# Kernel tuning notes

Hardware: AMD Instinct MI355X
Metric: run time of the kernel (lower is better)

The kernel has to match this reference:

```python
import jax, jax.numpy as jnp
import numpy as np


def setup_inputs() -> dict:
    key = jax.random.key(0)
    k1, k2 = jax.random.split(key)
    B, C, H, W = 16, 3, 512, 512
    predicted = jax.random.normal(k1, (B, C, H, W), dtype=jnp.float32)
    target = jax.random.randint(k2, (B, H, W), 0, 3, dtype=jnp.int32)
    return {"predicted": predicted, "target": target, "num_classes": 3}


def reference(predicted, target, num_classes):
    # predicted: [B, C, H, W] logits; target: [B, H, W] int labels
    B, C, H, W = predicted.shape
    smooth = 1.0

    # F.cross_entropy with default 'mean' reduction over all pixels
    logp = jax.nn.log_softmax(predicted, axis=1)           # [B,C,H,W]
    ce = -jnp.mean(jnp.take_along_axis(logp, target[:, None, :, :], axis=1))

    # Dice: the original casts softmax probs with .long() before summing,
    # which truncates toward zero (probs in [0,1) -> 0, exactly 1.0 -> 1).
    # We reproduce that faithfully with jnp.trunc.
    probs = jnp.exp(logp).reshape(B, C, H * W)             # softmax probs, [B,C,HW]
    tp = jnp.trunc(probs)                                   # faithful to .long() cast
    tgt = target.reshape(B, H * W)
    onehot = (tgt[:, None, :] == jnp.arange(num_classes)[None, :, None]).astype(probs.dtype)  # [B,nc,HW]

    intersection = jnp.sum(tp[:, :num_classes, :] * onehot, axis=-1)                 # [B,nc]
    union = jnp.sum(tp[:, :num_classes, :], axis=-1) + jnp.sum(onehot, axis=-1)      # [B,nc]
    coef = (2.0 * intersection + smooth) / (union + smooth)                           # [B,nc]
    batch_dice = jnp.mean(coef)  # mean over classes then batch == mean over both

    return ce + 1.0 - batch_dice
```

## Files before the change

### kernel.cpp

```cpp
#include <hip/hip_runtime.h>

constexpr int B_   = 16;
constexpr int C_   = 3;
constexpr int HW_  = 512 * 512;
constexpr int THREADS = 256;
constexpr int BLOCKS_PER_IMG = 128;
constexpr int NBLOCKS = B_ * BLOCKS_PER_IMG;
constexpr int F4_PER_BLOCK = HW_ / 4 / BLOCKS_PER_IMG;
constexpr int ITERS = F4_PER_BLOCK / THREADS;
constexpr int REC = 8;


__global__ __launch_bounds__(THREADS) void dice_ce_partial(
    const float* __restrict__ pred, const int* __restrict__ tgt,
    float* __restrict__ ws) {
  const int b = blockIdx.x / BLOCKS_PER_IMG;
  const int j = blockIdx.x % BLOCKS_PER_IMG;
  const int t = threadIdx.x;

  const float4* p0 = (const float4*)(pred + (size_t)b * C_ * HW_);
  const float4* p1 = (const float4*)(pred + (size_t)b * C_ * HW_ + HW_);
  const float4* p2 = (const float4*)(pred + (size_t)b * C_ * HW_ + 2 * HW_);
  const int4*   tg = (const int4*)(tgt + (size_t)b * HW_);

  float4 A0[ITERS], A1[ITERS], A2[ITERS];
  int4   T[ITERS];
#pragma unroll
  for (int i = 0; i < ITERS; ++i) {
    const int idx = j * F4_PER_BLOCK + i * THREADS + t;
    A0[i] = p0[idx];
    A1[i] = p1[idx];
    A2[i] = p2[idx];
    T[i]  = tg[idx];
  }

  float ce = 0.f;
  int pkA = 0, pkB = 0, pkC = 0, pkD = 0;

#pragma unroll
  for (int i = 0; i < ITERS; ++i) {
    float x0s[4] = {A0[i].x, A0[i].y, A0[i].z, A0[i].w};
    float x1s[4] = {A1[i].x, A1[i].y, A1[i].z, A1[i].w};
    float x2s[4] = {A2[i].x, A2[i].y, A2[i].z, A2[i].w};
    int   tvs[4] = {T[i].x, T[i].y, T[i].z, T[i].w};
#pragma unroll
    for (int k = 0; k < 4; ++k) {
      float x0 = x0s[k], x1 = x1s[k], x2 = x2s[k];
      int tv = tvs[k];
      float m  = fmaxf(x0, fmaxf(x1, x2));
      float e0 = __expf(x0 - m), e1 = __expf(x1 - m), e2 = __expf(x2 - m);
      float s  = e0 + e1 + e2;
      float ls = __logf(s);
      float xt = (tv == 0) ? x0 : ((tv == 1) ? x1 : x2);
      ce += (m + ls) - xt;
      int t0 = (e0 >= s) ? 1 : 0;
      int t1 = (e1 >= s) ? 1 : 0;
      int t2 = (e2 >= s) ? 1 : 0;
      pkA += ((tv == 1) ? 1 : 0) + ((tv == 2) ? (1 << 16) : 0);
      pkB += t0 + (t1 << 16);
      pkC += t2 + (((tv == 0) ? t0 : 0) << 16);
      pkD += ((tv == 1) ? t1 : 0) + (((tv == 2) ? t2 : 0) << 16);
    }
  }

  int pks[4] = {pkA, pkB, pkC, pkD};
#pragma unroll
  for (int off = 32; off > 0; off >>= 1) {
    ce += __shfl_down(ce, off, 64);
#pragma unroll
    for (int k = 0; k < 4; ++k) pks[k] += __shfl_down(pks[k], off, 64);
  }

  __shared__ float ceR[THREADS / 64];
  __shared__ int   pkR[THREADS / 64][4];
  const int wave = t >> 6, lane = t & 63;
  if (lane == 0) {
    ceR[wave] = ce;
#pragma unroll
    for (int k = 0; k < 4; ++k) pkR[wave][k] = pks[k];
  }
  __syncthreads();
  if (t == 0) {
#pragma unroll
    for (int w = 1; w < THREADS / 64; ++w) {
      ce += ceR[w];
#pragma unroll
      for (int k = 0; k < 4; ++k) pks[k] += pkR[w][k];
    }
    float4* rec = (float4*)(ws + (size_t)blockIdx.x * REC);
    rec[0] = make_float4(ce, __int_as_float(pks[0]), __int_as_float(pks[1]),
                         __int_as_float(pks[2]));
    rec[1] = make_float4(__int_as_float(pks[3]), 0.f, 0.f, 0.f);
  }
}

__global__ __launch_bounds__(1024) void dice_ce_final(
    const float* __restrict__ ws, float* __restrict__ out) {
  const int t = threadIdx.x;
  const int img = t >> 6;
  const int lane = t & 63;

  float ce = 0.f;
  float cnt1 = 0.f, cnt2 = 0.f;
  float tps0 = 0.f, tps1 = 0.f, tps2 = 0.f;
  float itr0 = 0.f, itr1 = 0.f, itr2 = 0.f;
#pragma unroll
  for (int r = 0; r < 2; ++r) {
    const int idx = img * BLOCKS_PER_IMG + r * 64 + lane;
    const float4* rec = (const float4*)(ws + (size_t)idx * REC);
    float4 r0 = rec[0], r1 = rec[1];
    ce += r0.x;
    int pA = __float_as_int(r0.y), pB = __float_as_int(r0.z);
    int pC = __float_as_int(r0.w), pD = __float_as_int(r1.x);
    cnt1 += (float)(pA & 0xffff); cnt2 += (float)(pA >> 16);
    tps0 += (float)(pB & 0xffff); tps1 += (float)(pB >> 16);
    tps2 += (float)(pC & 0xffff); itr0 += (float)(pC >> 16);
    itr1 += (float)(pD & 0xffff); itr2 += (float)(pD >> 16);
  }
  float v[9] = {ce, cnt1, cnt2, tps0, tps1, tps2, itr0, itr1, itr2};
#pragma unroll
  for (int k = 0; k < 9; ++k) {
#pragma unroll
    for (int off = 32; off > 0; off >>= 1) v[k] += __shfl_down(v[k], off, 64);
  }

  __shared__ float ceS[16];
  __shared__ float coefS[16];
  if (lane == 0) {
    float c1 = v[1], c2 = v[2];
    float c0 = (float)HW_ - c1 - c2;
    float coef = (2.f * v[6] + 1.f) / (v[3] + c0 + 1.f)
               + (2.f * v[7] + 1.f) / (v[4] + c1 + 1.f)
               + (2.f * v[8] + 1.f) / (v[5] + c2 + 1.f);
    ceS[img] = v[0];
    coefS[img] = coef;
  }
  __syncthreads();
  if (t == 0) {
    float cesum = 0.f, cf = 0.f;
#pragma unroll
    for (int i = 0; i < 16; ++i) { cesum += ceS[i]; cf += coefS[i]; }
    out[0] = cesum / ((float)B_ * (float)HW_) + 1.f - cf / (float)(B_ * C_);
  }
}

extern "C" void kernel_launch(void* const* d_in, const int* in_sizes, int n_in,
                              void* d_out, int out_size, void* d_ws, size_t ws_size,
                              hipStream_t stream) {
  const float* pred = (const float*)d_in[0];
  const int*   tgt  = (const int*)d_in[1];
  float*       out  = (float*)d_out;
  float*       ws   = (float*)d_ws;

  dice_ce_partial<<<NBLOCKS, THREADS, 0, stream>>>(pred, tgt, ws);
  dice_ce_final<<<1, 1024, 0, stream>>>(ws, out);
}
```

Before: 96.97 us.

## Fuse final reduction into main kernel via atomics and last-block ticket

Replaces the separate single-block finalize kernel with per-image atomic accumulators plus a ticket counter, so the last block to finish computes the loss. This removes one kernel launch and its gap. In exchange it adds a memset launch, a few thousand contended atomics, and threadfences. Float atomic accumulation of the CE sum makes the result order-dependent.

```diff
diff --git a/kernel.cpp b/kernel.cpp
--- a/kernel.cpp
+++ b/kernel.cpp
@@ -8,12 +8,14 @@
 constexpr int NBLOCKS = B_ * BLOCKS_PER_IMG;
 constexpr int F4_PER_BLOCK = HW_ / 4 / BLOCKS_PER_IMG;
 constexpr int ITERS = F4_PER_BLOCK / THREADS;
-constexpr int REC = 8;
 
+constexpr int ACC_STRIDE = 16;
+constexpr int CNT_SLOT = B_ * ACC_STRIDE;
+constexpr int WS_ZERO_BYTES = (CNT_SLOT + 16) * 4;
 
-__global__ __launch_bounds__(THREADS) void dice_ce_partial(
+__global__ __launch_bounds__(THREADS) void dice_ce_fused(
     const float* __restrict__ pred, const int* __restrict__ tgt,
-    float* __restrict__ ws) {
+    float* __restrict__ acc, float* __restrict__ out) {
   const int b = blockIdx.x / BLOCKS_PER_IMG;
   const int j = blockIdx.x % BLOCKS_PER_IMG;
   const int t = threadIdx.x;
@@ -73,6 +75,7 @@
 
   __shared__ float ceR[THREADS / 64];
   __shared__ int   pkR[THREADS / 64][4];
+  __shared__ int   lastFlag;
   const int wave = t >> 6, lane = t & 63;
   if (lane == 0) {
     ceR[wave] = ce;
@@ -87,60 +90,47 @@
 #pragma unroll
       for (int k = 0; k < 4; ++k) pks[k] += pkR[w][k];
     }
-    float4* rec = (float4*)(ws + (size_t)blockIdx.x * REC);
-    rec[0] = make_float4(ce, __int_as_float(pks[0]), __int_as_float(pks[1]),
-                         __int_as_float(pks[2]));
-    rec[1] = make_float4(__int_as_float(pks[3]), 0.f, 0.f, 0.f);
-  }
-}
-
-__global__ __launch_bounds__(1024) void dice_ce_final(
-    const float* __restrict__ ws, float* __restrict__ out) {
-  const int t = threadIdx.x;
-  const int img = t >> 6;
-  const int lane = t & 63;
-
-  float ce = 0.f;
-  float cnt1 = 0.f, cnt2 = 0.f;
-  float tps0 = 0.f, tps1 = 0.f, tps2 = 0.f;
-  float itr0 = 0.f, itr1 = 0.f, itr2 = 0.f;
-#pragma unroll
-  for (int r = 0; r < 2; ++r) {
-    const int idx = img * BLOCKS_PER_IMG + r * 64 + lane;
-    const float4* rec = (const float4*)(ws + (size_t)idx * REC);
-    float4 r0 = rec[0], r1 = rec[1];
-    ce += r0.x;
-    int pA = __float_as_int(r0.y), pB = __float_as_int(r0.z);
-    int pC = __float_as_int(r0.w), pD = __float_as_int(r1.x);
-    cnt1 += (float)(pA & 0xffff); cnt2 += (float)(pA >> 16);
-    tps0 += (float)(pB & 0xffff); tps1 += (float)(pB >> 16);
-    tps2 += (float)(pC & 0xffff); itr0 += (float)(pC >> 16);
-    itr1 += (float)(pD & 0xffff); itr2 += (float)(pD >> 16);
-  }
-  float v[9] = {ce, cnt1, cnt2, tps0, tps1, tps2, itr0, itr1, itr2};
-#pragma unroll
-  for (int k = 0; k < 9; ++k) {
-#pragma unroll
-    for (int off = 32; off > 0; off >>= 1) v[k] += __shfl_down(v[k], off, 64);
-  }
-
-  __shared__ float ceS[16];
-  __shared__ float coefS[16];
-  if (lane == 0) {
-    float c1 = v[1], c2 = v[2];
-    float c0 = (float)HW_ - c1 - c2;
-    float coef = (2.f * v[6] + 1.f) / (v[3] + c0 + 1.f)
-               + (2.f * v[7] + 1.f) / (v[4] + c1 + 1.f)
-               + (2.f * v[8] + 1.f) / (v[5] + c2 + 1.f);
-    ceS[img] = v[0];
-    coefS[img] = coef;
+    float* fa = acc + b * ACC_STRIDE;
+    int*   ia = (int*)fa;
+    atomicAdd(&fa[0], ce);
+    atomicAdd(&ia[1], pks[0] & 0xffff);
+    atomicAdd(&ia[2], pks[0] >> 16);
+    atomicAdd(&ia[3], pks[1] & 0xffff);
+    atomicAdd(&ia[4], pks[1] >> 16);
+    atomicAdd(&ia[5], pks[2] & 0xffff);
+    atomicAdd(&ia[6], pks[2] >> 16);
+    atomicAdd(&ia[7], pks[3] & 0xffff);
+    atomicAdd(&ia[8], pks[3] >> 16);
+    __threadfence();
+    int ticket = atomicAdd((int*)acc + CNT_SLOT, 1);
+    lastFlag = (ticket == NBLOCKS - 1) ? 1 : 0;
   }
   __syncthreads();
-  if (t == 0) {
-    float cesum = 0.f, cf = 0.f;
+
+  if (lastFlag && t < 64) {
+    __threadfence();
+    float cev = 0.f, coefv = 0.f;
+    if (t < B_) {
+      volatile float* fa = acc + t * ACC_STRIDE;
+      volatile int*   ia = (volatile int*)fa;
+      cev = fa[0];
+      float c1 = (float)ia[1], c2 = (float)ia[2];
+      float c0 = (float)HW_ - c1 - c2;
+      float tp0 = (float)ia[3], tp1 = (float)ia[4], tp2 = (float)ia[5];
+      float i0 = (float)ia[6], i1 = (float)ia[7], i2 = (float)ia[8];
+      coefv = (2.f * i0 + 1.f) / (tp0 + c0 + 1.f)
+            + (2.f * i1 + 1.f) / (tp1 + c1 + 1.f)
+            + (2.f * i2 + 1.f) / (tp2 + c2 + 1.f);
+    }
 #pragma unroll
-    for (int i = 0; i < 16; ++i) { cesum += ceS[i]; cf += coefS[i]; }
-    out[0] = cesum / ((float)B_ * (float)HW_) + 1.f - cf / (float)(B_ * C_);
+    for (int off = 8; off > 0; off >>= 1) {
+      cev   += __shfl_down(cev, off, 64);
+      coefv += __shfl_down(coefv, off, 64);
+    }
+    if (t == 0) {
+      out[0] = cev / ((float)B_ * (float)HW_) + 1.f
+             - coefv / (float)(B_ * C_);
+    }
   }
 }
 
@@ -152,6 +142,6 @@
   float*       out  = (float*)d_out;
   float*       ws   = (float*)d_ws;
 
-  dice_ce_partial<<<NBLOCKS, THREADS, 0, stream>>>(pred, tgt, ws);
-  dice_ce_final<<<1, 1024, 0, stream>>>(ws, out);
+  hipMemsetAsync(ws, 0, WS_ZERO_BYTES, stream);
+  dice_ce_fused<<<NBLOCKS, THREADS, 0, stream>>>(pred, tgt, ws, out);
 }
```

After: 164.9 us. +70.0%, slower.
